# Optimization experiments

Measured on AMD Instinct MI355X. Metric: run time of the kernel, lower is better.

Reference implementation:

```python
import jax, jax.numpy as jnp
import numpy as np

D = 1024      # neural_dim
M = 8192      # memory_size (assumed fully used)
H = 16        # num_heads
B = 64        # batch
HD = D // H   # head dim


def setup_inputs() -> dict:
    key = jax.random.key(0)
    ks = jax.random.split(key, 24)
    s = 0.02
    inp = {
        "neural_input": jax.random.normal(ks[0], (B, D), jnp.float32),
        "memory_keys": jax.random.normal(ks[1], (M, D), jnp.float32),
        "memory_values": jax.random.normal(ks[2], (M, D), jnp.float32),
        # query/key/value projections (nn.Linear weights are [out, in])
        "Wq": jax.random.normal(ks[3], (D, D), jnp.float32) * s,
        "bq": jnp.zeros((D,), jnp.float32),
        "Wk": jax.random.normal(ks[4], (D, D), jnp.float32) * s,
        "bk": jnp.zeros((D,), jnp.float32),
        "Wv": jax.random.normal(ks[5], (D, D), jnp.float32) * s,
        "bv": jnp.zeros((D,), jnp.float32),
        # MultiheadAttention packed in-projection [3D, D] and out projection
        "in_proj_w": jax.random.normal(ks[6], (3 * D, D), jnp.float32) * s,
        "in_proj_b": jnp.zeros((3 * D,), jnp.float32),
        "out_w": jax.random.normal(ks[7], (D, D), jnp.float32) * s,
        "out_b": jnp.zeros((D,), jnp.float32),
        # memory_gate: Linear(2D->D), ReLU, Linear(D->D), Sigmoid
        "gW1": jax.random.normal(ks[8], (D, 2 * D), jnp.float32) * s,
        "gb1": jnp.zeros((D,), jnp.float32),
        "gW2": jax.random.normal(ks[9], (D, D), jnp.float32) * s,
        "gb2": jnp.zeros((D,), jnp.float32),
        # integration: Linear(2D->2D), ReLU, Linear(2D->D)
        "iW1": jax.random.normal(ks[10], (2 * D, 2 * D), jnp.float32) * s,
        "ib1": jnp.zeros((2 * D,), jnp.float32),
        "iW2": jax.random.normal(ks[11], (D, 2 * D), jnp.float32) * s,
        "ib2": jnp.zeros((D,), jnp.float32),
    }
    return inp


def reference(neural_input, memory_keys, memory_values,
              Wq, bq, Wk, bk, Wv, bv,
              in_proj_w, in_proj_b, out_w, out_b,
              gW1, gb1, gW2, gb2, iW1, ib1, iW2, ib2):
    x = neural_input  # [B, D]
    # pre-projections (memory_used assumed all True -> full tables)
    q = x @ Wq.T + bq                  # [B, D]
    k = memory_keys @ Wk.T + bk        # [M, D]
    v = memory_values @ Wv.T + bv      # [M, D]

    # MultiheadAttention (single query per batch element; K/V shared
    # across batch instead of the redundant expand in the original)
    Wiq, Wik, Wiv = in_proj_w[:D], in_proj_w[D:2 * D], in_proj_w[2 * D:]
    biq, bik, biv = in_proj_b[:D], in_proj_b[D:2 * D], in_proj_b[2 * D:]
    qh = (q @ Wiq.T + biq).reshape(B, H, HD)   # [B, H, hd]
    kh = (k @ Wik.T + bik).reshape(M, H, HD)   # [M, H, hd]
    vh = (v @ Wiv.T + biv).reshape(M, H, HD)   # [M, H, hd]

    scale = 1.0 / np.sqrt(HD).astype(np.float32)
    scores = jnp.einsum('bhd,mhd->bhm', qh, kh) * scale  # [B, H, M]
    attn = jax.nn.softmax(scores, axis=-1)
    ctx = jnp.einsum('bhm,mhd->bhd', attn, vh).reshape(B, D)
    memory_signal = ctx @ out_w.T + out_b      # [B, D]

    # gated fusion
    gate_in = jnp.concatenate([x, memory_signal], axis=-1)          # [B, 2D]
    gate = jax.nn.sigmoid(jax.nn.relu(gate_in @ gW1.T + gb1) @ gW2.T + gb2)
    gated_memory = gate * memory_signal
    combined = jnp.concatenate([x, gated_memory], axis=-1)          # [B, 2D]
    out = jax.nn.relu(combined @ iW1.T + ib1) @ iW2.T + ib2         # [B, D]
    return out
```

## Files before the change

### kernel.cpp

```cpp
#include <hip/hip_runtime.h>
#include <hip/hip_bf16.h>
#include <stdint.h>


typedef __bf16 bf16;
typedef __bf16 bf16x4 __attribute__((ext_vector_type(4)));
typedef __bf16 bf16x8 __attribute__((ext_vector_type(8)));
typedef float f32x4 __attribute__((ext_vector_type(4)));

#define D_ 1024
#define M_ 8192
#define B_ 64
#define H_ 16

static __device__ __forceinline__ void gload16(const void* g, void* l) {
  __builtin_amdgcn_global_load_lds(
      (const __attribute__((address_space(1))) void*)g,
      (__attribute__((address_space(3))) void*)l, 16, 0, 0);
}

static __device__ __forceinline__ f32x4 mfma16(bf16x8 a, bf16x8 b, f32x4 c) {
  return __builtin_amdgcn_mfma_f32_16x16x32_bf16(a, b, c, 0, 0, 0);
}

struct CvtD { const float* src; bf16* dst; int end; };

template <int N>
static __device__ __forceinline__ void cvt_block(const CvtD* d, int b, int tid) {
  CvtD dd = d[N - 1];
  int begin = N > 1 ? d[N - 2].end : 0;
#pragma unroll
  for (int t = N - 2; t >= 0; t--)
    if (b < d[t].end) { dd = d[t]; begin = t ? d[t - 1].end : 0; }
  int64_t i = (int64_t)(b - begin) * 8192 + tid * 32;
  const float* src = dd.src + i;
  bf16* dst = dd.dst + i;
  float4 v[8];
#pragma unroll
  for (int u = 0; u < 8; u++) v[u] = *(const float4*)(src + u * 4);
#pragma unroll
  for (int u = 0; u < 8; u++) {
    bf16x4 o = { (bf16)v[u].x, (bf16)v[u].y, (bf16)v[u].z, (bf16)v[u].w };
    *(bf16x4*)(dst + u * 4) = o;
  }
}

template <int U, int KLEN, typename OutT>
__device__ __forceinline__ void thin_gemm(
    const bf16* __restrict__ A, int lda,
    const bf16* __restrict__ Bm, int ldb,
    OutT* __restrict__ C, int ldc,
    const float* __restrict__ bias, float scale) {
  const int tid = threadIdx.x, lane = tid & 63, w = tid >> 6;
  const int rl = lane & 15, qq = lane >> 4;
  const bf16* pa = A + (int64_t)(w * 16 + rl) * lda + qq * 8;
  const bf16* pb[4];
  pb[0] = Bm + (int64_t)rl * ldb + qq * 8;
  pb[1] = pb[0] + (int64_t)16 * ldb;
  pb[2] = pb[0] + (int64_t)32 * ldb;
  pb[3] = pb[0] + (int64_t)48 * ldb;
  f32x4 acc[4] = {};
  bf16x8 av[2][U], bv[2][U][4];
#pragma unroll
  for (int u = 0; u < U; u++) {
    av[0][u] = *(const bf16x8*)(pa + u * 32);
#pragma unroll
    for (int j = 0; j < 4; j++)
      bv[0][u][j] = *(const bf16x8*)(pb[j] + u * 32);
  }
  constexpr int NI = KLEN / (32 * U);
#pragma unroll
  for (int it = 0; it < NI; it++) {
    const int cur = it & 1, nxt = cur ^ 1;
    if (it + 1 < NI) {
      int k = (it + 1) * 32 * U;
#pragma unroll
      for (int u = 0; u < U; u++) {
        av[nxt][u] = *(const bf16x8*)(pa + k + u * 32);
#pragma unroll
        for (int j = 0; j < 4; j++)
          bv[nxt][u][j] = *(const bf16x8*)(pb[j] + k + u * 32);
      }
    }
#pragma unroll
    for (int u = 0; u < U; u++)
#pragma unroll
      for (int j = 0; j < 4; j++)
        acc[j] = mfma16(av[cur][u], bv[cur][u][j], acc[j]);
  }
#pragma unroll
  for (int j = 0; j < 4; j++) {
    int gn = j * 16 + rl;
    float bb = bias ? bias[gn] : 0.0f;
#pragma unroll
    for (int r = 0; r < 4; r++) {
      int gm = w * 16 + qq * 4 + r;
      C[(int64_t)gm * ldc + gn] = (OutT)((acc[j][r] + bb) * scale);
    }
  }
}

struct PrepArgs {
  CvtD d[2];
  const float *Wq, *Wk, *Wv, *inw, *inb, *bq, *bk, *bv;
  const float *outb, *gb1, *gb2, *ib1, *ib2;
  bf16* WT;
  float *bc, *msR, *g1R, *gateR, *h1R, *out, *Oraw, *lmat;
};

__global__ __launch_bounds__(256) void prep_kernel(PrepArgs a) {
  const int bx = blockIdx.x, tid = threadIdx.x;
  if (bx < 392) {
    cvt_block<2>(a.d, bx, tid);
  } else if (bx < 3464) {
    int t = bx - 392;
    int z = t >> 10, rem = t & 1023;
    const float* src = z == 0 ? a.Wq : z == 1 ? a.Wk : a.Wv;
    bf16* out = a.WT + (int64_t)z * D_ * D_;
    __shared__ bf16 tile[32][33];
    int tx = tid & 31, ty = tid >> 5;
    int r0 = (rem >> 5) * 32, c0 = (rem & 31) * 32;
#pragma unroll
    for (int i = 0; i < 32; i += 8)
      tile[ty + i][tx] = (bf16)src[(int64_t)(r0 + ty + i) * D_ + c0 + tx];
    __syncthreads();
#pragma unroll
    for (int i = 0; i < 32; i += 8)
      out[(int64_t)(c0 + ty + i) * D_ + r0 + tx] = tile[tx][ty + i];
  } else if (bx < 4232) {
    int t = bx - 3464;
    int w = tid >> 6, lane = tid & 63;
    int ng = t * 4 + w;
    int z = ng >> 10;
    const float* Wi = a.inw + (int64_t)ng * D_;
    const float* b = z == 0 ? a.bq : z == 1 ? a.bk : a.bv;
    float acc = 0.f;
#pragma unroll
    for (int l = 0; l < D_; l += 64) acc += Wi[l + lane] * b[l + lane];
#pragma unroll
    for (int m = 32; m; m >>= 1) acc += __shfl_xor(acc, m, 64);
    if (lane == 0) a.bc[ng] = acc + a.inb[ng];
  } else if (bx < 4616) {
    int t = bx - 4232;
    int seg = t >> 6, row = t & 63;
    int n = tid * 4;
    const float* b;
    float* dst;
    int bn = n;
    if (seg == 0)      { dst = a.msR   + row * 1024;        b = a.outb; }
    else if (seg == 1) { dst = a.g1R   + row * 1024;        b = a.gb1;  }
    else if (seg == 2) { dst = a.gateR + row * 1024;        b = a.gb2;  }
    else if (seg == 3) { dst = a.h1R   + row * 2048;        b = a.ib1;  }
    else if (seg == 4) { dst = a.h1R   + row * 2048 + 1024; b = a.ib1; bn = 1024 + n; }
    else               { dst = a.out   + row * 1024;        b = a.ib2;  }
    *(float4*)(dst + n) = *(const float4*)(b + bn);
  } else {
    int b = bx - 4616;
    float4 z4 = {0.f, 0.f, 0.f, 0.f};
    *(float4*)(a.Oraw + b * 1024 + tid * 4) = z4;
    if (b < 16 && tid < 64) a.lmat[b * 64 + tid] = 0.f;
  }
}

struct L2Args { CvtD d[7]; };

__global__ __launch_bounds__(256) void gemm_bigc(
    const bf16* __restrict__ A, const bf16* __restrict__ Bm,
    bf16* __restrict__ C, L2Args ca) {
  const int bid = blockIdx.x, tid = threadIdx.x;
  if (bid >= 192) {
    cvt_block<7>(ca.d, bid - 192, tid);
    return;
  }
  const int z = bid >> 6, r = bid & 63;
  const int m0 = (r >> 3) * 128, n0 = (r & 7) * 128;
  A += (int64_t)z * D_ * D_; Bm += (int64_t)z * D_ * D_;
  __shared__ alignas(16) bf16 As[128 * 32];
  __shared__ alignas(16) bf16 Bs[128 * 32];
  const int lane = tid & 63, w = tid >> 6;
  const int wm = (w & 1) * 64, wn = (w >> 1) * 64;
  const int rl = lane & 15, qq = lane >> 4;
  f32x4 acc[4][4] = {};

  int c0 = w * 64 + lane, c1 = (4 + w) * 64 + lane;
  int ra0 = c0 >> 2, qa0 = (c0 & 3) ^ ((ra0 >> 1) & 3);
  int ra1 = c1 >> 2, qa1 = (c1 & 3) ^ ((ra1 >> 1) & 3);
  const bf16* gA0 = A + (int64_t)(m0 + ra0) * D_ + qa0 * 8;
  const bf16* gA1 = A + (int64_t)(m0 + ra1) * D_ + qa1 * 8;
  const bf16* gB0 = Bm + (int64_t)(n0 + ra0) * D_ + qa0 * 8;
  const bf16* gB1 = Bm + (int64_t)(n0 + ra1) * D_ + qa1 * 8;
  bf16* lA0 = As + w * 512;
  bf16* lA1 = As + (4 + w) * 512;
  bf16* lB0 = Bs + w * 512;
  bf16* lB1 = Bs + (4 + w) * 512;

  for (int k0 = 0; k0 < D_; k0 += 32) {
    __syncthreads();
    gload16(gA0 + k0, lA0);
    gload16(gA1 + k0, lA1);
    gload16(gB0 + k0, lB0);
    gload16(gB1 + k0, lB1);
    __syncthreads();
    bf16x8 af[4], bb[4];
#pragma unroll
    for (int i = 0; i < 4; i++) {
      int rr = wm + i * 16 + rl;
      af[i] = *(const bf16x8*)(As + rr * 32 + (qq ^ ((rr >> 1) & 3)) * 8);
    }
#pragma unroll
    for (int j = 0; j < 4; j++) {
      int rr = wn + j * 16 + rl;
      bb[j] = *(const bf16x8*)(Bs + rr * 32 + (qq ^ ((rr >> 1) & 3)) * 8);
    }
#pragma unroll
    for (int i = 0; i < 4; i++)
#pragma unroll
      for (int j = 0; j < 4; j++)
        acc[i][j] = mfma16(af[i], bb[j], acc[i][j]);
  }
  C += (int64_t)z * D_ * D_;
#pragma unroll
  for (int j = 0; j < 4; j++) {
    int gn = n0 + wn + j * 16 + rl;
#pragma unroll
    for (int i = 0; i < 4; i++) {
      int gm0 = m0 + wm + i * 16 + qq * 4;
#pragma unroll
      for (int r2 = 0; r2 < 4; r2++)
        C[(int64_t)(gm0 + r2) * D_ + gn] = (bf16)acc[i][j][r2];
    }
  }
}

__global__ __launch_bounds__(512) void gemm256(
    const bf16* __restrict__ A,
    const bf16* __restrict__ Wc,
    const float* __restrict__ bc,
    bf16* __restrict__ kh, bf16* __restrict__ vhT,
    const bf16* __restrict__ qA, const bf16* __restrict__ qB,
    bf16* __restrict__ qC, const float* __restrict__ qbias) {
  extern __shared__ __align__(16) bf16 lds[];
  const int bid = blockIdx.x;
  if (bid >= 256) {
    if (threadIdx.x < 256) {
      int n0q = (bid - 256) * 64;
      thin_gemm<2, 1024, bf16>(qA, D_, qB + (int64_t)n0q * D_, D_,
                               qC + n0q, D_, qbias + n0q, 0.125f);
    }
    return;
  }
  const int lin = bid;
  const int xcd = lin & 7, s = lin >> 3;
  const int z = xcd >> 2;
  const int m0 = ((xcd & 3) * 8 + (s >> 2)) * 256;
  const int n0 = (s & 3) * 256;
  const bf16* Ab = A + (int64_t)z * M_ * D_;
  const bf16* Bb = Wc + (int64_t)(z + 1) * D_ * D_;
  const float* bias = bc + (z + 1) * D_;

  const int tid = threadIdx.x, lane = tid & 63, w = tid >> 6;
  const int rl = lane & 15, qq = lane >> 4;
  const int wr = w >> 2, wcn = w & 3;

  const int ci0 = w * 128 + lane, ci1 = ci0 + 64;
  const int ra0 = ci0 >> 2, ca0 = (ci0 & 3) ^ ((ra0 >> 1) & 3);
  const int ra1 = ci1 >> 2, ca1 = (ci1 & 3) ^ ((ra1 >> 1) & 3);
  const bf16* gA0 = Ab + (int64_t)(m0 + ra0) * D_ + ca0 * 8;
  const bf16* gA1 = Ab + (int64_t)(m0 + ra1) * D_ + ca1 * 8;
  const bf16* gB0 = Bb + (int64_t)(n0 + ra0) * D_ + ca0 * 8;
  const bf16* gB1 = Bb + (int64_t)(n0 + ra1) * D_ + ca1 * 8;
  const int lA0 = w * 1024, lA1 = lA0 + 512;

  f32x4 acc[8][4] = {};
  bf16x8 bfr[4], afr[4];
  const int sq8 = (qq ^ ((rl >> 1) & 3)) * 8;

#define SCB __builtin_amdgcn_sched_barrier(0)
#define BARR __builtin_amdgcn_s_barrier()
#define VMW(N) asm volatile("s_waitcnt vmcnt(" #N ")")

#define STAGE_FULL(BUF, KT)                          \
  do {                                               \
    bf16* bse_ = lds + (BUF) * 16384;                \
    gload16(gA0 + (KT) * 32, bse_ + lA0);            \
    gload16(gA1 + (KT) * 32, bse_ + lA1);            \
    gload16(gB0 + (KT) * 32, bse_ + 8192 + lA0);     \
    gload16(gB1 + (KT) * 32, bse_ + 8192 + lA1);     \
  } while (0)

#define PH_A(BUF, DOSTAGE, SKT)                                              \
  do {                                                                       \
    const bf16* ba_ = lds + (BUF) * 16384;                                   \
    const bf16* bb_ = ba_ + 8192;                                            \
    for (int j = 0; j < 4; j++)                                              \
      bfr[j] = *(const bf16x8*)(bb_ + (wcn * 64 + j * 16 + rl) * 32 + sq8);  \
    for (int mi = 0; mi < 4; mi++)                                           \
      afr[mi] = *(const bf16x8*)(ba_ + (wr * 128 + mi * 16 + rl) * 32 + sq8);\
    if (DOSTAGE) {                                                           \
      bf16* bse_ = lds + ((SKT) & 3) * 16384;                                \
      gload16(gA0 + (SKT) * 32, bse_ + lA0);                                 \
      gload16(gA1 + (SKT) * 32, bse_ + lA1);                                 \
    }                                                                        \
    SCB; BARR; SCB;                                                          \
    __builtin_amdgcn_s_setprio(1);                                           \
    for (int mi = 0; mi < 4; mi++)                                           \
      for (int j = 0; j < 4; j++)                                            \
        acc[mi][j] = mfma16(afr[mi], bfr[j], acc[mi][j]);                    \
    __builtin_amdgcn_s_setprio(0);                                           \
    SCB; BARR; SCB;                                                          \
  } while (0)

#define PH_B(BUF, DOSTAGE, SKT, VMSTMT)                                      \
  do {                                                                       \
    const bf16* ba_ = lds + (BUF) * 16384;                                   \
    for (int mi = 0; mi < 4; mi++)                                           \
      afr[mi] =                                                              \
          *(const bf16x8*)(ba_ + (wr * 128 + (mi + 4) * 16 + rl) * 32 + sq8);\
    if (DOSTAGE) {                                                           \
      bf16* bse_ = lds + ((SKT) & 3) * 16384;                                \
      gload16(gB0 + (SKT) * 32, bse_ + 8192 + lA0);                          \
      gload16(gB1 + (SKT) * 32, bse_ + 8192 + lA1);                          \
    }                                                                        \
    VMSTMT;                                                                  \
    SCB; BARR; SCB;                                                          \
    __builtin_amdgcn_s_setprio(1);                                           \
    for (int mi = 0; mi < 4; mi++)                                           \
      for (int j = 0; j < 4; j++)                                            \
        acc[mi + 4][j] = mfma16(afr[mi], bfr[j], acc[mi + 4][j]);            \
    __builtin_amdgcn_s_setprio(0);                                           \
    SCB; BARR; SCB;                                                          \
  } while (0)

  STAGE_FULL(0, 0);
  STAGE_FULL(1, 1);
  STAGE_FULL(2, 2);
  VMW(8);
  SCB; BARR; SCB;

#pragma unroll 1
  for (int t = 0; t < 7; t++) {
    const int kb = t * 4;
    PH_A(0, 1, kb + 3); PH_B(0, 1, kb + 3, VMW(8));
    PH_A(1, 1, kb + 4); PH_B(1, 1, kb + 4, VMW(8));
    PH_A(2, 1, kb + 5); PH_B(2, 1, kb + 5, VMW(8));
    PH_A(3, 1, kb + 6); PH_B(3, 1, kb + 6, VMW(8));
  }
  PH_A(0, 1, 31); PH_B(0, 1, 31, VMW(8));
  PH_A(1, 0, 0);  PH_B(1, 0, 0, VMW(4));
  PH_A(2, 0, 0);  PH_B(2, 0, 0, VMW(0));
  PH_A(3, 0, 0);  PH_B(3, 0, 0, (void)0);

#undef SCB
#undef BARR
#undef VMW
#undef STAGE_FULL
#undef PH_A
#undef PH_B

  if (z == 0) {
#pragma unroll
    for (int j = 0; j < 4; j++) {
      int gn = n0 + wcn * 64 + j * 16 + rl;
      float bb2 = bias[gn];
#pragma unroll
      for (int mi = 0; mi < 8; mi++) {
        int gm0 = m0 + wr * 128 + mi * 16 + qq * 4;
#pragma unroll
        for (int r = 0; r < 4; r++)
          kh[(int64_t)(gm0 + r) * D_ + gn] = (bf16)(acc[mi][j][r] + bb2);
      }
    }
  } else {
#pragma unroll
    for (int j = 0; j < 4; j++) {
      int gn = n0 + wcn * 64 + j * 16 + rl;
      float bb2 = bias[gn];
#pragma unroll
      for (int mi = 0; mi < 8; mi++) {
        int gm0 = m0 + wr * 128 + mi * 16 + qq * 4;
        f32x4 a = acc[mi][j];
        bf16x4 o = { (bf16)(a[0] + bb2), (bf16)(a[1] + bb2),
                     (bf16)(a[2] + bb2), (bf16)(a[3] + bb2) };
        *(bf16x4*)(vhT + (int64_t)gn * M_ + gm0) = o;
      }
    }
  }
}

__global__ __launch_bounds__(256, 2) void flash_kernel(
    const bf16* __restrict__ qh, const bf16* __restrict__ kh,
    const bf16* __restrict__ vhT, float* __restrict__ Oraw,
    float* __restrict__ lmat) {
  const int tid = threadIdx.x, lane = tid & 63, w = tid >> 6;
  const int rl = lane & 15, qq = lane >> 4;
  const int h = blockIdx.x >> 5, c = blockIdx.x & 31;
  __shared__ alignas(16) bf16 Plds[4 * 16 * 72];
  const bf16* qhp = qh + (int64_t)(w * 16 + rl) * D_ + h * 64 + qq * 8;
  bf16x8 aq0 = *(const bf16x8*)(qhp);
  bf16x8 aq1 = *(const bf16x8*)(qhp + 32);
  float lsum[4] = {0.f, 0.f, 0.f, 0.f};
  f32x4 acc_o[4] = {};
  bf16* pl = Plds + w * 1152;
  const bf16* khb = kh + (int64_t)(c * 256) * D_ + h * 64 + qq * 8;
  const bf16* vtb = vhT + (int64_t)(h * 64) * M_ + c * 256 + qq * 8;
  for (int nt = 0; nt < 4; nt++) {
    int mb = nt * 64;
    bf16x8 bk0[4], bk1[4], vv0[4], vv1[4];
#pragma unroll
    for (int j = 0; j < 4; j++) {
      const bf16* p = khb + (int64_t)(mb + j * 16 + rl) * D_;
      bk0[j] = *(const bf16x8*)(p);
      bk1[j] = *(const bf16x8*)(p + 32);
      const bf16* q = vtb + (int64_t)(j * 16 + rl) * M_ + mb;
      vv0[j] = *(const bf16x8*)(q);
      vv1[j] = *(const bf16x8*)(q + 32);
    }
    f32x4 s[4] = {};
#pragma unroll
    for (int j = 0; j < 4; j++) {
      s[j] = mfma16(aq0, bk0[j], s[j]);
      s[j] = mfma16(aq1, bk1[j], s[j]);
    }
#pragma unroll
    for (int j = 0; j < 4; j++)
#pragma unroll
      for (int r = 0; r < 4; r++) {
        float p = __expf(s[j][r]);
        lsum[r] += p;
        pl[(qq * 4 + r) * 72 + j * 16 + rl] = (bf16)p;
      }
    bf16x8 pa0 = *(const bf16x8*)(pl + rl * 72 + qq * 8);
    bf16x8 pa1 = *(const bf16x8*)(pl + rl * 72 + 32 + qq * 8);
#pragma unroll
    for (int j = 0; j < 4; j++) {
      acc_o[j] = mfma16(pa0, vv0[j], acc_o[j]);
      acc_o[j] = mfma16(pa1, vv1[j], acc_o[j]);
    }
  }
#pragma unroll
  for (int msk = 1; msk <= 8; msk <<= 1)
#pragma unroll
    for (int r = 0; r < 4; r++) lsum[r] += __shfl_xor(lsum[r], msk, 64);
#pragma unroll
  for (int j = 0; j < 4; j++)
#pragma unroll
    for (int r = 0; r < 4; r++)
      atomicAdd(&Oraw[(int64_t)(w * 16 + qq * 4 + r) * D_ + h * 64 + j * 16 + rl],
                acc_o[j][r]);
  if (rl == 0)
#pragma unroll
    for (int r = 0; r < 4; r++)
      atomicAdd(&lmat[h * 64 + w * 16 + qq * 4 + r], lsum[r]);
}

struct Chunk { const void* p0; const void* p1; int ld; int kind; };
struct StageArgs { Chunk c[16]; };

template <int NKK>
__global__ __launch_bounds__(256) void tail_stage(
    StageArgs sa, const bf16* __restrict__ Bw, int ldb,
    float* __restrict__ Craw, int ldc) {
  const int n0 = blockIdx.x * 64, kc = blockIdx.y;
  const int bk0 = kc * NKK * 32;
  const Chunk ch = sa.c[kc];
  const int tid = threadIdx.x, lane = tid & 63, w = tid >> 6;
  const int rl = lane & 15, qq = lane >> 4;
  const int m = w * 16 + rl;
  const bf16* pb[4];
#pragma unroll
  for (int j = 0; j < 4; j++)
    pb[j] = Bw + (int64_t)(n0 + j * 16 + rl) * ldb + bk0 + qq * 8;
  f32x4 acc[4] = {};
#pragma unroll
  for (int kk = 0; kk < NKK; kk++) {
    bf16x8 af;
    if (ch.kind == 0) {
      af = *(const bf16x8*)((const bf16*)ch.p0 + (int64_t)m * ch.ld +
                            kk * 32 + qq * 8);
    } else {
      const float* p = (const float*)ch.p0 + (int64_t)m * ch.ld + kk * 32 + qq * 8;
      float4 u0 = *(const float4*)p;
      float4 u1 = *(const float4*)(p + 4);
      if (ch.kind == 2) {
        u0.x = fmaxf(u0.x, 0.f); u0.y = fmaxf(u0.y, 0.f);
        u0.z = fmaxf(u0.z, 0.f); u0.w = fmaxf(u0.w, 0.f);
        u1.x = fmaxf(u1.x, 0.f); u1.y = fmaxf(u1.y, 0.f);
        u1.z = fmaxf(u1.z, 0.f); u1.w = fmaxf(u1.w, 0.f);
      } else if (ch.kind == 3) {
        const float* pm = (const float*)ch.p1 + (int64_t)m * ch.ld + kk * 32 + qq * 8;
        float4 m0 = *(const float4*)pm;
        float4 m1 = *(const float4*)(pm + 4);
        u0.x = m0.x / (1.f + __expf(-u0.x)); u0.y = m0.y / (1.f + __expf(-u0.y));
        u0.z = m0.z / (1.f + __expf(-u0.z)); u0.w = m0.w / (1.f + __expf(-u0.w));
        u1.x = m1.x / (1.f + __expf(-u1.x)); u1.y = m1.y / (1.f + __expf(-u1.y));
        u1.z = m1.z / (1.f + __expf(-u1.z)); u1.w = m1.w / (1.f + __expf(-u1.w));
      } else if (ch.kind == 4) {
        int hidx = (bk0 + kk * 32) >> 6;
        float linv = 1.0f / ((const float*)ch.p1)[hidx * 64 + m];
        u0.x *= linv; u0.y *= linv; u0.z *= linv; u0.w *= linv;
        u1.x *= linv; u1.y *= linv; u1.z *= linv; u1.w *= linv;
      }
      af = (bf16x8){ (bf16)u0.x, (bf16)u0.y, (bf16)u0.z, (bf16)u0.w,
                     (bf16)u1.x, (bf16)u1.y, (bf16)u1.z, (bf16)u1.w };
    }
    bf16x8 bf_[4];
#pragma unroll
    for (int j = 0; j < 4; j++) bf_[j] = *(const bf16x8*)(pb[j] + kk * 32);
#pragma unroll
    for (int j = 0; j < 4; j++) acc[j] = mfma16(af, bf_[j], acc[j]);
  }
#pragma unroll
  for (int j = 0; j < 4; j++) {
    int gn = n0 + j * 16 + rl;
#pragma unroll
    for (int r = 0; r < 4; r++) {
      int gm = w * 16 + qq * 4 + r;
      atomicAdd(&Craw[(int64_t)gm * ldc + gn], acc[j][r]);
    }
  }
}

extern "C" void kernel_launch(void* const* d_in, const int* in_sizes, int n_in,
                              void* d_out, int out_size, void* d_ws,
                              size_t ws_size, hipStream_t stream) {
  (void)in_sizes; (void)n_in; (void)out_size;
  const float* x    = (const float*)d_in[0];
  const float* mk   = (const float*)d_in[1];
  const float* mv   = (const float*)d_in[2];
  const float* Wq   = (const float*)d_in[3];
  const float* bq   = (const float*)d_in[4];
  const float* Wk   = (const float*)d_in[5];
  const float* bk   = (const float*)d_in[6];
  const float* Wv   = (const float*)d_in[7];
  const float* bv   = (const float*)d_in[8];
  const float* inw  = (const float*)d_in[9];
  const float* inb  = (const float*)d_in[10];
  const float* outw = (const float*)d_in[11];
  const float* outb = (const float*)d_in[12];
  const float* gW1  = (const float*)d_in[13];
  const float* gb1  = (const float*)d_in[14];
  const float* gW2  = (const float*)d_in[15];
  const float* gb2  = (const float*)d_in[16];
  const float* iW1  = (const float*)d_in[17];
  const float* ib1  = (const float*)d_in[18];
  const float* iW2  = (const float*)d_in[19];
  const float* ib2  = (const float*)d_in[20];

  char* ws = (char*)d_ws;
  size_t off = 0;
  auto alloc = [&](size_t bytes) {
    char* p = ws + off;
    off += (bytes + 255) & ~(size_t)255;
    return p;
  };
  bf16* mkmv  = (bf16*)alloc((size_t)2 * M_ * D_ * 2);
  bf16* inpj  = (bf16*)alloc((size_t)3 * D_ * D_ * 2);
  bf16* WT    = (bf16*)alloc((size_t)3 * D_ * D_ * 2);
  bf16* Wc    = (bf16*)alloc((size_t)3 * D_ * D_ * 2);
  float* bc   = (float*)alloc(3 * D_ * 4);
  bf16* xbf   = (bf16*)alloc((size_t)B_ * D_ * 2);
  bf16* qh    = (bf16*)alloc((size_t)B_ * D_ * 2);
  bf16* kh    = (bf16*)alloc((size_t)M_ * D_ * 2);
  bf16* vhT   = (bf16*)alloc((size_t)M_ * D_ * 2);
  float* Oraw = (float*)alloc((size_t)B_ * D_ * 4);
  float* lmat = (float*)alloc((size_t)H_ * B_ * 4);
  float* msR  = (float*)alloc((size_t)B_ * D_ * 4);
  float* g1R  = (float*)alloc((size_t)B_ * D_ * 4);
  float* gateR= (float*)alloc((size_t)B_ * D_ * 4);
  float* h1R  = (float*)alloc((size_t)B_ * 2 * D_ * 4);
  bf16* gW1b  = (bf16*)alloc((size_t)D_ * 2 * D_ * 2);
  bf16* gW2b  = (bf16*)alloc((size_t)D_ * D_ * 2);
  bf16* iW1b  = (bf16*)alloc((size_t)2 * D_ * 2 * D_ * 2);
  bf16* iW2b  = (bf16*)alloc((size_t)D_ * 2 * D_ * 2);
  bf16* outwb = (bf16*)alloc((size_t)D_ * D_ * 2);
  if (ws_size < off) return;

  PrepArgs pa;
  pa.d[0] = { inw, inpj, 384 };
  pa.d[1] = { x,   xbf,  392 };
  pa.Wq = Wq; pa.Wk = Wk; pa.Wv = Wv; pa.inw = inw; pa.inb = inb;
  pa.bq = bq; pa.bk = bk; pa.bv = bv;
  pa.outb = outb; pa.gb1 = gb1; pa.gb2 = gb2; pa.ib1 = ib1; pa.ib2 = ib2;
  pa.WT = WT; pa.bc = bc; pa.msR = msR; pa.g1R = g1R; pa.gateR = gateR;
  pa.h1R = h1R; pa.out = (float*)d_out; pa.Oraw = Oraw; pa.lmat = lmat;
  prep_kernel<<<dim3(4680), 256, 0, stream>>>(pa);

  L2Args ca;
  ca.d[0] = { mk,   mkmv,           1024 };
  ca.d[1] = { mv,   mkmv + M_ * D_, 2048 };
  ca.d[2] = { gW1,  gW1b,           2304 };
  ca.d[3] = { gW2,  gW2b,           2432 };
  ca.d[4] = { iW1,  iW1b,           2944 };
  ca.d[5] = { iW2,  iW2b,           3200 };
  ca.d[6] = { outw, outwb,          3328 };
  gemm_bigc<<<dim3(3520), 256, 0, stream>>>(inpj, WT, Wc, ca);

  hipFuncSetAttribute((const void*)gemm256,
                      hipFuncAttributeMaxDynamicSharedMemorySize, 131072);
  gemm256<<<dim3(272), dim3(512), 131072, stream>>>(
      mkmv, Wc, bc, kh, vhT, xbf, Wc, qh, bc);

  flash_kernel<<<dim3(512), 256, 0, stream>>>(qh, kh, vhT, Oraw, lmat);

  StageArgs s1;
  for (int kc = 0; kc < 8; kc++) s1.c[kc] = { Oraw + kc * 128, lmat, D_, 4 };
  tail_stage<4><<<dim3(16, 8), 256, 0, stream>>>(s1, outwb, D_, msR, D_);

  StageArgs s2;
  for (int kc = 0; kc < 8; kc++)  s2.c[kc] = { xbf + kc * 128, nullptr, D_, 0 };
  for (int kc = 8; kc < 16; kc++) s2.c[kc] = { msR + (kc - 8) * 128, nullptr, D_, 1 };
  tail_stage<4><<<dim3(16, 16), 256, 0, stream>>>(s2, gW1b, 2 * D_, g1R, D_);

  StageArgs s3;
  for (int kc = 0; kc < 8; kc++) s3.c[kc] = { g1R + kc * 128, nullptr, D_, 2 };
  tail_stage<4><<<dim3(16, 8), 256, 0, stream>>>(s3, gW2b, D_, gateR, D_);

  StageArgs s4;
  for (int kc = 0; kc < 8; kc++)  s4.c[kc] = { xbf + kc * 128, nullptr, D_, 0 };
  for (int kc = 8; kc < 16; kc++)
    s4.c[kc] = { gateR + (kc - 8) * 128, msR + (kc - 8) * 128, D_, 3 };
  tail_stage<4><<<dim3(32, 16), 256, 0, stream>>>(s4, iW1b, 2 * D_, h1R, 2 * D_);

  StageArgs s5;
  for (int kc = 0; kc < 16; kc++) s5.c[kc] = { h1R + kc * 128, nullptr, 2 * D_, 2 };
  tail_stage<4><<<dim3(16, 16), 256, 0, stream>>>(s5, iW2b, 2 * D_,
                                                  (float*)d_out, D_);
}
```

Measured before the change: 334.0 us.

## Split-K weight-combine GEMM with atomics, compute q via two thin GEMMs

The combined-weight GEMMs (Wik·Wk, Wiv·Wv) are split into four K-chunks with fp32 atomicAdd into a zeroed scratch buffer, then converted to bf16 by a new kernel, giving 512 blocks instead of 192. The Wq·Wiq combine is removed. The query is instead computed as x·Wq^T followed by a thin GEMM with Wiq. The intent is to fill the GPU better during the weight-combine phase and skip a full 1024^3 GEMM. In exchange it adds fp32 atomics traffic, an extra conversion kernel, and aliases the scratch buffer onto kh.

```diff
diff --git a/kernel.cpp b/kernel.cpp
--- a/kernel.cpp
+++ b/kernel.cpp
@@ -101,22 +101,22 @@
 }
 
 struct PrepArgs {
-  CvtD d[2];
-  const float *Wq, *Wk, *Wv, *inw, *inb, *bq, *bk, *bv;
+  CvtD d[3];
+  const float *Wk, *Wv, *inw, *inb, *bq, *bk, *bv;
   const float *outb, *gb1, *gb2, *ib1, *ib2;
   bf16* WT;
-  float *bc, *msR, *g1R, *gateR, *h1R, *out, *Oraw, *lmat;
+  float *bc, *msR, *g1R, *gateR, *h1R, *out, *Oraw, *lmat, *Wcp;
 };
 
 __global__ __launch_bounds__(256) void prep_kernel(PrepArgs a) {
   const int bx = blockIdx.x, tid = threadIdx.x;
-  if (bx < 392) {
-    cvt_block<2>(a.d, bx, tid);
-  } else if (bx < 3464) {
-    int t = bx - 392;
+  if (bx < 520) {
+    cvt_block<3>(a.d, bx, tid);
+  } else if (bx < 2568) {
+    int t = bx - 520;
     int z = t >> 10, rem = t & 1023;
-    const float* src = z == 0 ? a.Wq : z == 1 ? a.Wk : a.Wv;
-    bf16* out = a.WT + (int64_t)z * D_ * D_;
+    const float* src = z == 0 ? a.Wk : a.Wv;
+    bf16* out = a.WT + (int64_t)(z + 1) * D_ * D_;
     __shared__ bf16 tile[32][33];
     int tx = tid & 31, ty = tid >> 5;
     int r0 = (rem >> 5) * 32, c0 = (rem & 31) * 32;
@@ -127,8 +127,8 @@
 #pragma unroll
     for (int i = 0; i < 32; i += 8)
       out[(int64_t)(c0 + ty + i) * D_ + r0 + tx] = tile[tx][ty + i];
-  } else if (bx < 4232) {
-    int t = bx - 3464;
+  } else if (bx < 3336) {
+    int t = bx - 2568;
     int w = tid >> 6, lane = tid & 63;
     int ng = t * 4 + w;
     int z = ng >> 10;
@@ -140,8 +140,8 @@
 #pragma unroll
     for (int m = 32; m; m >>= 1) acc += __shfl_xor(acc, m, 64);
     if (lane == 0) a.bc[ng] = acc + a.inb[ng];
-  } else if (bx < 4616) {
-    int t = bx - 4232;
+  } else if (bx < 3720) {
+    int t = bx - 3336;
     int seg = t >> 6, row = t & 63;
     int n = tid * 4;
     const float* b;
@@ -154,27 +154,43 @@
     else if (seg == 4) { dst = a.h1R   + row * 2048 + 1024; b = a.ib1; bn = 1024 + n; }
     else               { dst = a.out   + row * 1024;        b = a.ib2;  }
     *(float4*)(dst + n) = *(const float4*)(b + bn);
-  } else {
-    int b = bx - 4616;
+  } else if (bx < 3784) {
+    int b = bx - 3720;
     float4 z4 = {0.f, 0.f, 0.f, 0.f};
     *(float4*)(a.Oraw + b * 1024 + tid * 4) = z4;
     if (b < 16 && tid < 64) a.lmat[b * 64 + tid] = 0.f;
+  } else {
+    int b = bx - 3784;
+    float4 z4 = {0.f, 0.f, 0.f, 0.f};
+    float* p = a.Wcp + (int64_t)b * 4096 + tid * 16;
+#pragma unroll
+    for (int u = 0; u < 4; u++) *(float4*)(p + u * 4) = z4;
   }
 }
 
 struct L2Args { CvtD d[7]; };
 
-__global__ __launch_bounds__(256) void gemm_bigc(
-    const bf16* __restrict__ A, const bf16* __restrict__ Bm,
-    bf16* __restrict__ C, L2Args ca) {
+__global__ __launch_bounds__(256) void gemm_l2c(
+    const bf16* __restrict__ inpj, const bf16* __restrict__ WT,
+    float* __restrict__ Wcp, const bf16* __restrict__ xbf,
+    const bf16* __restrict__ Wqb, bf16* __restrict__ q1, L2Args ca) {
   const int bid = blockIdx.x, tid = threadIdx.x;
-  if (bid >= 192) {
-    cvt_block<7>(ca.d, bid - 192, tid);
+  if (bid >= 528) {
+    cvt_block<7>(ca.d, bid - 528, tid);
     return;
   }
-  const int z = bid >> 6, r = bid & 63;
-  const int m0 = (r >> 3) * 128, n0 = (r & 7) * 128;
-  A += (int64_t)z * D_ * D_; Bm += (int64_t)z * D_ * D_;
+  if (bid >= 512) {
+    int n0q = (bid - 512) * 64;
+    thin_gemm<2, 1024, bf16>(xbf, D_, Wqb + (int64_t)n0q * D_, D_,
+                             q1 + n0q, D_, nullptr, 1.0f);
+    return;
+  }
+  const int z = bid >> 8, kc = (bid >> 6) & 3, tile = bid & 63;
+  const int m0 = (tile >> 3) * 128, n0 = (tile & 7) * 128;
+  const bf16* A = inpj + (int64_t)(z + 1) * D_ * D_ + kc * 256;
+  const bf16* Bm = WT + (int64_t)(z + 1) * D_ * D_ + kc * 256;
+  float* C = Wcp + (int64_t)z * D_ * D_;
+
   __shared__ alignas(16) bf16 As[128 * 32];
   __shared__ alignas(16) bf16 Bs[128 * 32];
   const int lane = tid & 63, w = tid >> 6;
@@ -194,7 +210,7 @@
   bf16* lB0 = Bs + w * 512;
   bf16* lB1 = Bs + (4 + w) * 512;
 
-  for (int k0 = 0; k0 < D_; k0 += 32) {
+  for (int k0 = 0; k0 < 256; k0 += 32) {
     __syncthreads();
     gload16(gA0 + k0, lA0);
     gload16(gA1 + k0, lA1);
@@ -218,7 +234,6 @@
       for (int j = 0; j < 4; j++)
         acc[i][j] = mfma16(af[i], bb[j], acc[i][j]);
   }
-  C += (int64_t)z * D_ * D_;
 #pragma unroll
   for (int j = 0; j < 4; j++) {
     int gn = n0 + wn + j * 16 + rl;
@@ -227,9 +242,18 @@
       int gm0 = m0 + wm + i * 16 + qq * 4;
 #pragma unroll
       for (int r2 = 0; r2 < 4; r2++)
-        C[(int64_t)(gm0 + r2) * D_ + gn] = (bf16)acc[i][j][r2];
-    }
-  }
+        atomicAdd(&C[(int64_t)(gm0 + r2) * D_ + gn], acc[i][j][r2]);
+    }
+  }
+}
+
+__global__ __launch_bounds__(256) void cvt_wc(
+    const float* __restrict__ Wcp, bf16* __restrict__ Wc) {
+  const int z = blockIdx.x >> 10, b = blockIdx.x & 1023;
+  const int i = (b * 256 + threadIdx.x) * 4;
+  float4 s = *(const float4*)(Wcp + (int64_t)z * D_ * D_ + i);
+  bf16x4 o = { (bf16)s.x, (bf16)s.y, (bf16)s.z, (bf16)s.w };
+  *(bf16x4*)(Wc + (int64_t)(z + 1) * D_ * D_ + i) = o;
 }
 
 __global__ __launch_bounds__(512) void gemm256(
@@ -573,17 +597,22 @@
   bf16* iW1b  = (bf16*)alloc((size_t)2 * D_ * 2 * D_ * 2);
   bf16* iW2b  = (bf16*)alloc((size_t)D_ * 2 * D_ * 2);
   bf16* outwb = (bf16*)alloc((size_t)D_ * D_ * 2);
+  bf16* Wqb   = (bf16*)alloc((size_t)D_ * D_ * 2);
+  bf16* q1    = (bf16*)alloc((size_t)B_ * D_ * 2);
   if (ws_size < off) return;
+  float* Wcp = (float*)kh;
 
   PrepArgs pa;
   pa.d[0] = { inw, inpj, 384 };
   pa.d[1] = { x,   xbf,  392 };
-  pa.Wq = Wq; pa.Wk = Wk; pa.Wv = Wv; pa.inw = inw; pa.inb = inb;
+  pa.d[2] = { Wq,  Wqb,  520 };
+  pa.Wk = Wk; pa.Wv = Wv; pa.inw = inw; pa.inb = inb;
   pa.bq = bq; pa.bk = bk; pa.bv = bv;
   pa.outb = outb; pa.gb1 = gb1; pa.gb2 = gb2; pa.ib1 = ib1; pa.ib2 = ib2;
   pa.WT = WT; pa.bc = bc; pa.msR = msR; pa.g1R = g1R; pa.gateR = gateR;
   pa.h1R = h1R; pa.out = (float*)d_out; pa.Oraw = Oraw; pa.lmat = lmat;
-  prep_kernel<<<dim3(4680), 256, 0, stream>>>(pa);
+  pa.Wcp = Wcp;
+  prep_kernel<<<dim3(4296), 256, 0, stream>>>(pa);
 
   L2Args ca;
   ca.d[0] = { mk,   mkmv,           1024 };
@@ -593,12 +622,14 @@
   ca.d[4] = { iW1,  iW1b,           2944 };
   ca.d[5] = { iW2,  iW2b,           3200 };
   ca.d[6] = { outw, outwb,          3328 };
-  gemm_bigc<<<dim3(3520), 256, 0, stream>>>(inpj, WT, Wc, ca);
+  gemm_l2c<<<dim3(3856), 256, 0, stream>>>(inpj, WT, Wcp, xbf, Wqb, q1, ca);
+
+  cvt_wc<<<dim3(2048), 256, 0, stream>>>(Wcp, Wc);
 
   hipFuncSetAttribute((const void*)gemm256,
                       hipFuncAttributeMaxDynamicSharedMemorySize, 131072);
   gemm256<<<dim3(272), dim3(512), 131072, stream>>>(
-      mkmv, Wc, bc, kh, vhT, xbf, Wc, qh, bc);
+      mkmv, Wc, bc, kh, vhT, q1, inpj, qh, bc);
 
   flash_kernel<<<dim3(512), 256, 0, stream>>>(qh, kh, vhT, Oraw, lmat);
 
```

Measured after the change: 355.0 us. +6.3%, slower.
